# Optimization experiments

Measured on AMD Instinct MI355X. Metric: run time of the kernel, lower is better.

Reference implementation:

```python
import jax, jax.numpy as jnp
import numpy as np

NUM_HEADS = 4   # num_heads init kwarg
KERNEL = 7      # kernel_size init kwarg
EPS = 1e-5      # nn.LayerNorm default eps


def setup_inputs() -> dict:
    key = jax.random.key(0)
    ks = jax.random.split(key, 6)
    C, depth = 128, 2
    x = jax.random.normal(ks[0], (2, C, 64, 64), jnp.float32)
    qkv_w = jax.random.normal(ks[1], (depth, 3 * C, C), jnp.float32) * 0.05
    qkv_b = jnp.zeros((depth, 3 * C), jnp.float32)
    rpb = jax.random.normal(ks[2], (depth, NUM_HEADS, 2 * KERNEL - 1, 2 * KERNEL - 1), jnp.float32) * 0.02
    proj_w = jax.random.normal(ks[3], (depth, C, C), jnp.float32) * 0.05
    proj_b = jnp.zeros((depth, C), jnp.float32)
    ln_g = jnp.ones((C,), jnp.float32)
    ln_b = jnp.zeros((C,), jnp.float32)
    return dict(x=x, qkv_w=qkv_w, qkv_b=qkv_b, rpb=rpb,
                proj_w=proj_w, proj_b=proj_b, ln_g=ln_g, ln_b=ln_b)


def _na2d(x, w_qkv, b_qkv, rpb, w_p, b_p):
    """NATTEN-style 2D neighborhood attention. x: (B,H,W,C)."""
    B, H, W, C = x.shape
    h, k = NUM_HEADS, KERNEL
    d = C // h
    qkv = (x @ w_qkv.T + b_qkv).reshape(B, H, W, 3, h, d)
    q = qkv[..., 0, :, :] * (d ** -0.5)   # (B,H,W,h,d)
    kk = qkv[..., 1, :, :]
    v = qkv[..., 2, :, :]
    # edge-clamped window starts: each query sees exactly k x k neighbors
    si = jnp.clip(jnp.arange(H) - k // 2, 0, H - k)
    sj = jnp.clip(jnp.arange(W) - k // 2, 0, W - k)
    idx_i = si[:, None] + jnp.arange(k)   # (H,k) absolute row indices
    idx_j = sj[:, None] + jnp.arange(k)   # (W,k) absolute col indices

    def win(t):  # (B,H,W,h,d) -> (B,H,W,k,k,h,d)
        t = t[:, idx_i]          # (B,H,k,W,h,d)
        t = t[:, :, :, idx_j]    # (B,H,k,W,k,h,d)
        return jnp.transpose(t, (0, 1, 3, 2, 4, 5, 6))

    kw = win(kk)
    vw = win(v)
    attn = jnp.einsum('bijhd,bijpqhd->bijhpq', q, kw)  # (B,H,W,h,k,k)
    # relative position bias: index = (neighbor_abs - query) + (k-1)
    bi = jnp.arange(k)[None, :] + (k - 1) - (jnp.arange(H) - si)[:, None]  # (H,k)
    bj = jnp.arange(k)[None, :] + (k - 1) - (jnp.arange(W) - sj)[:, None]  # (W,k)
    bias = rpb[:, bi[:, None, :, None], bj[None, :, None, :]]  # (h,H,W,k,k)
    attn = attn + jnp.transpose(bias, (1, 2, 0, 3, 4))[None]
    attn = jax.nn.softmax(attn.reshape(B, H, W, h, k * k), axis=-1).reshape(B, H, W, h, k, k)
    out = jnp.einsum('bijhpq,bijpqhd->bijhd', attn, vw).reshape(B, H, W, C)
    return out @ w_p.T + b_p


def reference(x, qkv_w, qkv_b, rpb, proj_w, proj_b, ln_g, ln_b):
    y = jnp.transpose(x, (0, 2, 3, 1))  # NCHW -> NHWC
    for l in range(qkv_w.shape[0]):     # depth=2 stacked NA layers
        y = _na2d(y, qkv_w[l], qkv_b[l], rpb[l], proj_w[l], proj_b[l])
    mu = y.mean(-1, keepdims=True)
    var = y.var(-1, keepdims=True)
    y = (y - mu) / jnp.sqrt(var + EPS) * ln_g + ln_b
    return jnp.transpose(y, (0, 3, 1, 2))  # NHWC -> NCHW
```

## Files before the change

### kernel.cpp

```cpp
#include <hip/hip_runtime.h>
#include <hip/hip_bf16.h>
#include <math.h>

#define PIX 8192
typedef __hip_bfloat16 bf16;
typedef __attribute__((ext_vector_type(8))) short short8;
typedef __attribute__((ext_vector_type(4))) float f32x4;

__device__ inline float bflo(unsigned u) { return __uint_as_float(u << 16); }
__device__ inline float bfhi(unsigned u) { return __uint_as_float(u & 0xffff0000u); }
__device__ inline unsigned short f2b(float f) {
  __hip_bfloat16 h = __float2bfloat16(f);
  return *reinterpret_cast<unsigned short*>(&h);
}
__device__ inline unsigned pack2(float a, float b) {
  return (unsigned)f2b(a) | ((unsigned)f2b(b) << 16);
}
__device__ inline short8 ldw8(const float* __restrict__ p) {
  f32x4 lo = *(const f32x4*)p;
  f32x4 hi = *(const f32x4*)(p + 4);
  short8 r;
  r[0] = (short)f2b(lo[0]); r[1] = (short)f2b(lo[1]);
  r[2] = (short)f2b(lo[2]); r[3] = (short)f2b(lo[3]);
  r[4] = (short)f2b(hi[0]); r[5] = (short)f2b(hi[1]);
  r[6] = (short)f2b(hi[2]); r[7] = (short)f2b(hi[3]);
  return r;
}

__global__ __launch_bounds__(256) void xqkv_cvt(const float* __restrict__ x,
                                                const float* __restrict__ qw,
                                                const float* __restrict__ qb,
                                                unsigned short* __restrict__ qkv,
                                                const float* __restrict__ pw,
                                                unsigned short* __restrict__ wq1,
                                                unsigned short* __restrict__ wp) {
  if (blockIdx.x >= 512) {
    int idx = (blockIdx.x - 512) * 256 + threadIdx.x;
    wq1[idx] = f2b(qw[49152 + idx]);
    wq1[idx + 16384] = f2b(qw[49152 + idx + 16384]);
    if (idx < 16384) wq1[idx + 32768] = f2b(qw[49152 + idx + 32768]);
    wp[idx] = f2b(pw[idx]);
    return;
  }

  __shared__ __align__(16) unsigned short As[16 * 136];
  int m0 = blockIdx.x * 16;
  int tid = threadIdx.x;
  int b = m0 >> 12, i = (m0 >> 6) & 63, j0 = m0 & 63;

  for (int idx = tid; idx < 2048; idx += 256) {
    int c = idx >> 4, jl = idx & 15;
    As[jl * 136 + c] =
        f2b(x[(size_t)b * 524288 + (size_t)c * 4096 + i * 64 + j0 + jl]);
  }
  __syncthreads();

  int w = tid >> 6, lane = tid & 63;
  int quad = lane >> 4, l16 = lane & 15;
  short8 a[4];
#pragma unroll
  for (int kc = 0; kc < 4; ++kc)
    a[kc] = *(const short8*)(As + l16 * 136 + kc * 32 + quad * 8);
#pragma unroll
  for (int nt = 0; nt < 6; ++nt) {
    int col = w * 96 + nt * 16 + l16;
    const float* wrow = qw + (size_t)col * 128 + quad * 8;
    f32x4 c = {0.f, 0.f, 0.f, 0.f};
#pragma unroll
    for (int kc = 0; kc < 4; ++kc)
      c = __builtin_amdgcn_mfma_f32_16x16x32_bf16(a[kc], ldw8(wrow + kc * 32), c, 0, 0, 0);
    float bv = qb[col];
#pragma unroll
    for (int r2 = 0; r2 < 4; ++r2)
      qkv[(size_t)(m0 + quad * 4 + r2) * 384 + col] = f2b(c[r2] + bv);
  }
}

__global__ __launch_bounds__(256) void gemm_mfma(const unsigned short* __restrict__ A,
                                                 const unsigned short* __restrict__ W,
                                                 const float* __restrict__ bias,
                                                 unsigned short* __restrict__ Cmat,
                                                 int N) {
  int m0 = blockIdx.x * 64, n0 = blockIdx.y * 64;
  int tid = threadIdx.x;
  int w = tid >> 6, lane = tid & 63;
  int quad = lane >> 4, l16 = lane & 15;

  const short8* ap =
      (const short8*)(A + (size_t)(m0 + w * 16 + l16) * 128 + quad * 8);
  short8 a[4];
#pragma unroll
  for (int kc = 0; kc < 4; ++kc) a[kc] = ap[kc * 4];

  f32x4 acc[4];
#pragma unroll
  for (int nt = 0; nt < 4; ++nt) {
    const short8* bp =
        (const short8*)(W + (size_t)(n0 + nt * 16 + l16) * 128 + quad * 8);
    f32x4 c = {0.f, 0.f, 0.f, 0.f};
#pragma unroll
    for (int kc = 0; kc < 4; ++kc)
      c = __builtin_amdgcn_mfma_f32_16x16x32_bf16(a[kc], bp[kc * 4], c, 0, 0, 0);
    acc[nt] = c;
  }

#pragma unroll
  for (int nt = 0; nt < 4; ++nt) {
    int col = n0 + nt * 16 + l16;
    float bv = bias[col];
#pragma unroll
    for (int r = 0; r < 4; ++r) {
      int m = m0 + w * 16 + quad * 4 + r;
      Cmat[(size_t)m * N + col] = f2b(acc[nt][r] + bv);
    }
  }
}

#define RSTRIDE 72
__global__ __launch_bounds__(256, 2) void na_attn(const unsigned short* __restrict__ qkvp,
                                                  const float* __restrict__ rpb,
                                                  unsigned short* __restrict__ out) {
  __shared__ __align__(16) unsigned short kbuf[140 * RSTRIDE];
  __shared__ __align__(16) unsigned short vbuf[140 * RSTRIDE];
  __shared__ float rb[338];
  __shared__ float sc[64][52];

  int ti = blockIdx.x >> 4, tj = blockIdx.x & 15;
  int hp = blockIdx.y;
  int bz = blockIdx.z;
  int tid = threadIdx.x;
  int bi0 = ti * 8 - 3, bj0 = tj * 4 - 3;

  for (int t = tid; t < 338; t += 256) rb[t] = rpb[hp * 338 + t];

  for (int t = tid; t < 2240; t += 256) {
    int row = t >> 4;
    int sub = t & 15;
    int isv = sub >> 3;
    int c = sub & 7;
    int ri = row / 10, rj = row - ri * 10;
    int gi = bi0 + ri, gj = bj0 + rj;
    uint4 val = make_uint4(0, 0, 0, 0);
    if ((unsigned)gi < 64u && (unsigned)gj < 64u) {
      int pixn = (bz * 64 + gi) * 64 + gj;
      val = *(const uint4*)(qkvp + (size_t)pixn * 384 + 128 + isv * 128 +
                            hp * 64 + c * 8);
    }
    *(uint4*)((isv ? vbuf : kbuf) + row * RSTRIDE + c * 8) = val;
  }
  __syncthreads();

  int r = tid & 3;
  int hl = (tid >> 2) & 1;
  int px = tid >> 3;
  int ph = px * 2 + hl;
  int pi = px >> 2, pj = px & 3;
  int i = ti * 8 + pi, j = tj * 4 + pj;
  int si = min(max(i - 3, 0), 57), sj = min(max(j - 3, 0), 57);
  int li = si - bi0, lj = sj - bj0;
  int oi = i - si, oj = j - sj;
  int H = hp * 2 + hl;
  int pix = (bz * 64 + i) * 64 + j;

  const float scale = 0.17677669529663687f;
  float q[8];
  {
    uint4 t = *(const uint4*)(qkvp + (size_t)pix * 384 + H * 32 + r * 8);
    q[0] = bflo(t.x) * scale;  q[1] = bfhi(t.x) * scale;
    q[2] = bflo(t.y) * scale;  q[3] = bfhi(t.y) * scale;
    q[4] = bflo(t.z) * scale;  q[5] = bfhi(t.z) * scale;
    q[6] = bflo(t.w) * scale;  q[7] = bfhi(t.w) * scale;
  }

  const unsigned short* kh = kbuf + hl * 32 + r * 8;
  const unsigned short* vh = vbuf + hl * 32 + r * 8;
  const float* rbh = rb + hl * 169;

#pragma unroll
  for (int p = 0; p < 7; ++p) {
#pragma unroll
    for (int qq = 0; qq < 7; ++qq) {
      int n = (li + p) * 10 + (lj + qq);
      uint4 t = *(const uint4*)(kh + n * RSTRIDE);
      float dot = q[0] * bflo(t.x) + q[1] * bfhi(t.x)
                + q[2] * bflo(t.y) + q[3] * bfhi(t.y)
                + q[4] * bflo(t.z) + q[5] * bfhi(t.z)
                + q[6] * bflo(t.w) + q[7] * bfhi(t.w);
      dot += __shfl_xor(dot, 1);
      dot += __shfl_xor(dot, 2);
      if (r == 0) sc[ph][p * 7 + qq] = dot + rbh[(p + 6 - oi) * 13 + (qq + 6 - oj)];
    }
  }
  __syncthreads();

  float m = -INFINITY;
#pragma unroll
  for (int n = 0; n < 49; ++n) m = fmaxf(m, sc[ph][n]);

  float sum = 0.f;
  float acc[8] = {0.f, 0.f, 0.f, 0.f, 0.f, 0.f, 0.f, 0.f};
#pragma unroll
  for (int p = 0; p < 7; ++p) {
#pragma unroll
    for (int qq = 0; qq < 7; ++qq) {
      float e = __expf(sc[ph][p * 7 + qq] - m);
      sum += e;
      int n = (li + p) * 10 + (lj + qq);
      uint4 t = *(const uint4*)(vh + n * RSTRIDE);
      acc[0] += e * bflo(t.x);  acc[1] += e * bfhi(t.x);
      acc[2] += e * bflo(t.y);  acc[3] += e * bfhi(t.y);
      acc[4] += e * bflo(t.z);  acc[5] += e * bfhi(t.z);
      acc[6] += e * bflo(t.w);  acc[7] += e * bfhi(t.w);
    }
  }
  float inv = 1.f / sum;
  uint4 t;
  t.x = pack2(acc[0] * inv, acc[1] * inv);
  t.y = pack2(acc[2] * inv, acc[3] * inv);
  t.z = pack2(acc[4] * inv, acc[5] * inv);
  t.w = pack2(acc[6] * inv, acc[7] * inv);
  *(uint4*)(out + (size_t)pix * 128 + H * 32 + r * 8) = t;
}

__global__ __launch_bounds__(256) void ln_out(const unsigned short* __restrict__ y,
                                              const float* __restrict__ g,
                                              const float* __restrict__ bta,
                                              float* __restrict__ out) {
  __shared__ float tile[64][129];
  __shared__ float mean_s[64], rstd_s[64];
  int blk = blockIdx.x;
  int b = blk >> 6, i = blk & 63;
  int tid = threadIdx.x;
  const unsigned short* yrow = y + (size_t)blk * 64 * 128;
  for (int idx = tid; idx < 8192; idx += 256) {
    int j = idx >> 7, c = idx & 127;
    tile[j][c] = __uint_as_float((unsigned)yrow[idx] << 16);
  }
  __syncthreads();
  int jj = tid >> 2, qtr = tid & 3;
  float sum = 0.f, sumsq = 0.f;
#pragma unroll
  for (int cc = 0; cc < 32; ++cc) {
    float v = tile[jj][qtr * 32 + cc];
    sum += v; sumsq += v * v;
  }
  sum += __shfl_xor(sum, 1);  sum += __shfl_xor(sum, 2);
  sumsq += __shfl_xor(sumsq, 1);  sumsq += __shfl_xor(sumsq, 2);
  if (qtr == 0) {
    float mu = sum * (1.f / 128.f);
    mean_s[jj] = mu;
    rstd_s[jj] = rsqrtf(sumsq * (1.f / 128.f) - mu * mu + 1e-5f);
  }
  __syncthreads();
  int c0 = tid >> 6;
  int j = tid & 63;
  for (int c = c0; c < 128; c += 4) {
    float v = (tile[j][c] - mean_s[j]) * rstd_s[j] * g[c] + bta[c];
    out[(((size_t)b * 128 + c) * 64 + i) * 64 + j] = v;
  }
}

extern "C" void kernel_launch(void* const* d_in, const int* in_sizes, int n_in,
                              void* d_out, int out_size, void* d_ws, size_t ws_size,
                              hipStream_t stream) {
  (void)in_sizes; (void)n_in; (void)out_size; (void)ws_size;
  const float* x   = (const float*)d_in[0];
  const float* qw  = (const float*)d_in[1];
  const float* qb  = (const float*)d_in[2];
  const float* rpb = (const float*)d_in[3];
  const float* pw  = (const float*)d_in[4];
  const float* pb  = (const float*)d_in[5];
  const float* lg  = (const float*)d_in[6];
  const float* lb  = (const float*)d_in[7];

  unsigned short* y    = (unsigned short*)d_ws;
  unsigned short* qkv  = y + (size_t)PIX * 128;
  unsigned short* wq1  = qkv + (size_t)PIX * 384;
  unsigned short* wp   = wq1 + 49152;
  unsigned short* attn = (unsigned short*)d_out;
  float* out = (float*)d_out;

  xqkv_cvt<<<640, 256, 0, stream>>>(x, qw, qb, qkv, pw, wq1, wp);
  na_attn<<<dim3(128, 2, 2), 256, 0, stream>>>(qkv, rpb, attn);
  gemm_mfma<<<dim3(128, 2), 256, 0, stream>>>(attn, wp, pb, y, 128);
  gemm_mfma<<<dim3(128, 6), 256, 0, stream>>>(y, wq1, qb + 384, qkv, 384);
  na_attn<<<dim3(128, 2, 2), 256, 0, stream>>>(qkv, rpb + 676, attn);
  gemm_mfma<<<dim3(128, 2), 256, 0, stream>>>(attn, wp + 16384, pb + 128, y, 128);
  ln_out<<<128, 256, 0, stream>>>(y, lg, lb, out);
}
```

Measured before the change: 147.8 us.

## Fuse neighborhood attention with output projection GEMM per tile

```diff
diff --git a/kernel.cpp b/kernel.cpp
--- a/kernel.cpp
+++ b/kernel.cpp
@@ -116,65 +116,64 @@
   }
 }
 
-#define RSTRIDE 72
-__global__ __launch_bounds__(256, 2) void na_attn(const unsigned short* __restrict__ qkvp,
-                                                  const float* __restrict__ rpb,
-                                                  unsigned short* __restrict__ out) {
+#define RSTRIDE 136
+__global__ __launch_bounds__(512, 1) void attnproj(const unsigned short* __restrict__ qkvp,
+                                                   const float* __restrict__ rpb,
+                                                   const unsigned short* __restrict__ wp,
+                                                   const float* __restrict__ pbias,
+                                                   unsigned short* __restrict__ y) {
   __shared__ __align__(16) unsigned short kbuf[140 * RSTRIDE];
   __shared__ __align__(16) unsigned short vbuf[140 * RSTRIDE];
-  __shared__ float rb[338];
-  __shared__ float sc[64][52];
+  __shared__ float rb[676];
+  __shared__ float sc[128][52];
 
   int ti = blockIdx.x >> 4, tj = blockIdx.x & 15;
-  int hp = blockIdx.y;
-  int bz = blockIdx.z;
+  int bz = blockIdx.y;
   int tid = threadIdx.x;
   int bi0 = ti * 8 - 3, bj0 = tj * 4 - 3;
 
-  for (int t = tid; t < 338; t += 256) rb[t] = rpb[hp * 338 + t];
-
-  for (int t = tid; t < 2240; t += 256) {
-    int row = t >> 4;
-    int sub = t & 15;
-    int isv = sub >> 3;
-    int c = sub & 7;
+  for (int t = tid; t < 676; t += 512) rb[t] = rpb[t];
+
+  for (int t = tid; t < 4480; t += 512) {
+    int row = t >> 5;
+    int sub = t & 31;
+    int isv = sub >> 4;
+    int c = sub & 15;
     int ri = row / 10, rj = row - ri * 10;
     int gi = bi0 + ri, gj = bj0 + rj;
     uint4 val = make_uint4(0, 0, 0, 0);
     if ((unsigned)gi < 64u && (unsigned)gj < 64u) {
       int pixn = (bz * 64 + gi) * 64 + gj;
-      val = *(const uint4*)(qkvp + (size_t)pixn * 384 + 128 + isv * 128 +
-                            hp * 64 + c * 8);
+      val = *(const uint4*)(qkvp + (size_t)pixn * 384 + 128 + isv * 128 + c * 8);
     }
     *(uint4*)((isv ? vbuf : kbuf) + row * RSTRIDE + c * 8) = val;
   }
   __syncthreads();
 
   int r = tid & 3;
-  int hl = (tid >> 2) & 1;
-  int px = tid >> 3;
-  int ph = px * 2 + hl;
+  int hh = (tid >> 2) & 3;
+  int px = tid >> 4;
+  int ph = px * 4 + hh;
   int pi = px >> 2, pj = px & 3;
   int i = ti * 8 + pi, j = tj * 4 + pj;
   int si = min(max(i - 3, 0), 57), sj = min(max(j - 3, 0), 57);
   int li = si - bi0, lj = sj - bj0;
   int oi = i - si, oj = j - sj;
-  int H = hp * 2 + hl;
   int pix = (bz * 64 + i) * 64 + j;
 
   const float scale = 0.17677669529663687f;
   float q[8];
   {
-    uint4 t = *(const uint4*)(qkvp + (size_t)pix * 384 + H * 32 + r * 8);
+    uint4 t = *(const uint4*)(qkvp + (size_t)pix * 384 + hh * 32 + r * 8);
     q[0] = bflo(t.x) * scale;  q[1] = bfhi(t.x) * scale;
     q[2] = bflo(t.y) * scale;  q[3] = bfhi(t.y) * scale;
     q[4] = bflo(t.z) * scale;  q[5] = bfhi(t.z) * scale;
     q[6] = bflo(t.w) * scale;  q[7] = bfhi(t.w) * scale;
   }
 
-  const unsigned short* kh = kbuf + hl * 32 + r * 8;
-  const unsigned short* vh = vbuf + hl * 32 + r * 8;
-  const float* rbh = rb + hl * 169;
+  const unsigned short* kh = kbuf + hh * 32 + r * 8;
+  const unsigned short* vh = vbuf + hh * 32 + r * 8;
+  const float* rbh = rb + hh * 169;
 
 #pragma unroll
   for (int p = 0; p < 7; ++p) {
@@ -219,7 +218,34 @@
   t.y = pack2(acc[2] * inv, acc[3] * inv);
   t.z = pack2(acc[4] * inv, acc[5] * inv);
   t.w = pack2(acc[6] * inv, acc[7] * inv);
-  *(uint4*)(out + (size_t)pix * 128 + H * 32 + r * 8) = t;
+  unsigned short* obuf = kbuf;
+  *(uint4*)(obuf + px * RSTRIDE + hh * 32 + r * 8) = t;
+  __syncthreads();
+
+  int w = tid >> 6, lane = tid & 63;
+  int quad = lane >> 4, l16 = lane & 15;
+  int mt = w & 1;
+  int ng = w >> 1;
+  short8 a[4];
+#pragma unroll
+  for (int kc = 0; kc < 4; ++kc)
+    a[kc] = *(const short8*)(obuf + (mt * 16 + l16) * RSTRIDE + kc * 32 + quad * 8);
+#pragma unroll
+  for (int s = 0; s < 2; ++s) {
+    int col = (ng * 2 + s) * 16 + l16;
+    const short8* bp = (const short8*)(wp + (size_t)col * 128 + quad * 8);
+    f32x4 c = {0.f, 0.f, 0.f, 0.f};
+#pragma unroll
+    for (int kc = 0; kc < 4; ++kc)
+      c = __builtin_amdgcn_mfma_f32_16x16x32_bf16(a[kc], bp[kc * 4], c, 0, 0, 0);
+    float bv = pbias[col];
+#pragma unroll
+    for (int r2 = 0; r2 < 4; ++r2) {
+      int mloc = mt * 16 + quad * 4 + r2;
+      int gpix = (bz * 64 + ti * 8 + (mloc >> 2)) * 64 + tj * 4 + (mloc & 3);
+      y[(size_t)gpix * 128 + col] = f2b(c[r2] + bv);
+    }
+  }
 }
 
 __global__ __launch_bounds__(256) void ln_out(const unsigned short* __restrict__ y,
@@ -232,17 +258,18 @@
   int b = blk >> 6, i = blk & 63;
   int tid = threadIdx.x;
   const unsigned short* yrow = y + (size_t)blk * 64 * 128;
-  for (int idx = tid; idx < 8192; idx += 256) {
-    int j = idx >> 7, c = idx & 127;
-    tile[j][c] = __uint_as_float((unsigned)yrow[idx] << 16);
-  }
-  __syncthreads();
   int jj = tid >> 2, qtr = tid & 3;
   float sum = 0.f, sumsq = 0.f;
 #pragma unroll
-  for (int cc = 0; cc < 32; ++cc) {
-    float v = tile[jj][qtr * 32 + cc];
-    sum += v; sumsq += v * v;
+  for (int u = 0; u < 4; ++u) {
+    int c = qtr * 32 + u * 8;
+    uint4 t = *(const uint4*)(yrow + jj * 128 + c);
+    float v0 = bflo(t.x), v1 = bfhi(t.x), v2 = bflo(t.y), v3 = bfhi(t.y);
+    float v4 = bflo(t.z), v5 = bfhi(t.z), v6 = bflo(t.w), v7 = bfhi(t.w);
+    sum += v0 + v1 + v2 + v3 + v4 + v5 + v6 + v7;
+    sumsq += v0*v0 + v1*v1 + v2*v2 + v3*v3 + v4*v4 + v5*v5 + v6*v6 + v7*v7;
+    tile[jj][c+0] = v0; tile[jj][c+1] = v1; tile[jj][c+2] = v2; tile[jj][c+3] = v3;
+    tile[jj][c+4] = v4; tile[jj][c+5] = v5; tile[jj][c+6] = v6; tile[jj][c+7] = v7;
   }
   sum += __shfl_xor(sum, 1);  sum += __shfl_xor(sum, 2);
   sumsq += __shfl_xor(sumsq, 1);  sumsq += __shfl_xor(sumsq, 2);
@@ -277,14 +304,11 @@
   unsigned short* qkv  = y + (size_t)PIX * 128;
   unsigned short* wq1  = qkv + (size_t)PIX * 384;
   unsigned short* wp   = wq1 + 49152;
-  unsigned short* attn = (unsigned short*)d_out;
   float* out = (float*)d_out;
 
   xqkv_cvt<<<640, 256, 0, stream>>>(x, qw, qb, qkv, pw, wq1, wp);
-  na_attn<<<dim3(128, 2, 2), 256, 0, stream>>>(qkv, rpb, attn);
-  gemm_mfma<<<dim3(128, 2), 256, 0, stream>>>(attn, wp, pb, y, 128);
+  attnproj<<<dim3(128, 2), 512, 0, stream>>>(qkv, rpb, wp, pb, y);
   gemm_mfma<<<dim3(128, 6), 256, 0, stream>>>(y, wq1, qb + 384, qkv, 384);
-  na_attn<<<dim3(128, 2, 2), 256, 0, stream>>>(qkv, rpb + 676, attn);
-  gemm_mfma<<<dim3(128, 2), 256, 0, stream>>>(attn, wp + 16384, pb + 128, y, 128);
+  attnproj<<<dim3(128, 2), 512, 0, stream>>>(qkv, rpb + 676, wp + 16384, pb + 128, y);
   ln_out<<<128, 256, 0, stream>>>(y, lg, lb, out);
 }
```

Measured after the change: 139.1 us. -5.9%, faster.
